# Performance work log

Hardware: AMD Instinct MI355X
Metric: run time of the kernel (lower is better)

Reference implementation:

```python
import jax, jax.numpy as jnp
import numpy as np

B, S, D = 4, 2048, 1024


def setup_inputs() -> dict:
    key = jax.random.key(0)
    k1, k2, k3, k4 = jax.random.split(key, 4)
    x = jax.random.normal(k1, (B, S, D), dtype=jnp.float32)
    # 'random_normal' keras initializer uses stddev=0.05
    w_keys = jax.random.normal(k2, (D, D), dtype=jnp.float32) * 0.05
    w_queries = jax.random.normal(k3, (D, D), dtype=jnp.float32) * 0.05
    w_values = jax.random.normal(k4, (D, D), dtype=jnp.float32) * 0.05
    return {"x": x, "w_keys": w_keys, "w_queries": w_queries, "w_values": w_values}


def reference(x, w_keys, w_queries, w_values):
    # fact = sqrt(input feature dim)
    fact = jnp.sqrt(jnp.asarray(x.shape[-1], x.dtype))
    vk = x @ w_keys      # [B,S,D]
    vq = x @ w_queries   # [B,S,D]
    vv = x @ w_values    # [B,S,D]
    # NOTE: module computes K @ Q^T (keys as rows), softmax over last axis
    kq = jnp.einsum('bsd,btd->bst', vk, vq) / fact   # [B,S,S]
    sn = jax.nn.softmax(kq, axis=-1)
    # pm + transpose_b cancel: out = sn @ vv
    out = jnp.einsum('bst,btd->bsd', sn, vv)         # [B,S,D]
    return out
```

## Files before the change

kernel.cpp:

```cpp
#include <hip/hip_runtime.h>


typedef __attribute__((ext_vector_type(8))) short bf16x8;
typedef __attribute__((ext_vector_type(4))) float f32x4;

__device__ __forceinline__ unsigned short f2bf(float f) {
    unsigned int u = __float_as_uint(f);
    u += 0x7fff + ((u >> 16) & 1);
    return (unsigned short)(u >> 16);
}
__device__ __forceinline__ float bf2f(unsigned short s) {
    return __uint_as_float((unsigned int)s << 16);
}

__device__ __forceinline__ void gld_lds16(const unsigned short* g, unsigned short* l) {
    __builtin_amdgcn_global_load_lds(
        (const __attribute__((address_space(1))) void*)g,
        (__attribute__((address_space(3))) void*)l, 16, 0, 0);
}

template<int N> __device__ __forceinline__ void vmcnt_wait() {
    if constexpr (N == 0) asm volatile("s_waitcnt vmcnt(0)" ::: "memory");
    else if constexpr (N == 8) asm volatile("s_waitcnt vmcnt(8)" ::: "memory");
}
__device__ __forceinline__ void bar() {
    asm volatile("" ::: "memory");
    __builtin_amdgcn_s_barrier();
    asm volatile("" ::: "memory");
}

template<int KT, bool RS>
__device__ __forceinline__ void gemm4(
    const unsigned short* __restrict__ A, const unsigned short* __restrict__ B,
    int lda, int ldb, int bm, int bn,
    unsigned short* As, unsigned short* Bs,
    f32x4 (&acc)[4][4], float (&rs)[4])
{
    const int tid  = threadIdx.x;
    const int lane = tid & 63;
    const int wave = tid >> 6;
    const int wr = wave >> 1, wc = wave & 1;
    const int lr = lane & 15, kg = lane >> 4;

    const int srow = tid >> 2;
    const int ssrc = ((tid & 3) ^ ((tid >> 3) & 3)) * 8;
    const unsigned short* pa0 = A + (size_t)(bm + srow) * lda + ssrc;
    const unsigned short* pa1 = A + (size_t)(bm + 64 + srow) * lda + ssrc;
    const unsigned short* pb0 = B + (size_t)(bn + srow) * ldb + ssrc;
    const unsigned short* pb1 = B + (size_t)(bn + 64 + srow) * ldb + ssrc;

    const int phys = (kg ^ ((lr >> 1) & 3)) * 8;
    const int aoff = (wr * 64 + lr) * 32 + phys;
    const int boff = (wc * 64 + lr) * 32 + phys;

    auto stage = [&](int buf, int kt) {
        unsigned short* da = As + buf * 8192 + wave * 512;
        unsigned short* db = Bs + buf * 8192 + wave * 512;
        #pragma unroll
        for (int kh = 0; kh < 2; kh++) {
            const int go = kt * 64 + kh * 32;
            gld_lds16(pa0 + go, da + kh * 4096);
            gld_lds16(pa1 + go, da + kh * 4096 + 2048);
            gld_lds16(pb0 + go, db + kh * 4096);
            gld_lds16(pb1 + go, db + kh * 4096 + 2048);
        }
    };

    stage(0, 0);
    stage(1, 1);
    vmcnt_wait<8>();
    bar();

    for (int kt = 0; kt < KT; ++kt) {
        const int c = kt & 1;
        const unsigned short* Ab = As + c * 8192 + aoff;
        const unsigned short* Bb = Bs + c * 8192 + boff;

        #pragma unroll
        for (int kh = 0; kh < 2; kh++) {
            bf16x8 af[4], bf[4];
            #pragma unroll
            for (int mf = 0; mf < 4; mf++)
                af[mf] = *reinterpret_cast<const bf16x8*>(Ab + kh * 4096 + mf * 512);
            #pragma unroll
            for (int nf = 0; nf < 4; nf++)
                bf[nf] = *reinterpret_cast<const bf16x8*>(Bb + kh * 4096 + nf * 512);
            __builtin_amdgcn_s_setprio(1);
            #pragma unroll
            for (int mf = 0; mf < 4; mf++)
                #pragma unroll
                for (int nf = 0; nf < 4; nf++)
                    acc[mf][nf] = __builtin_amdgcn_mfma_f32_16x16x32_bf16(af[mf], bf[nf], acc[mf][nf], 0, 0, 0);
            __builtin_amdgcn_s_setprio(0);
            if constexpr (RS) {
                #pragma unroll
                for (int mf = 0; mf < 4; mf++)
                    #pragma unroll
                    for (int e = 0; e < 8; e++) rs[mf] += bf2f(((unsigned short*)&af[mf])[e]);
            }
        }

        if (kt == KT - 1) break;
        bar();
        if (kt + 2 < KT) {
            stage(c, kt + 2);
            vmcnt_wait<8>();
        } else {
            vmcnt_wait<0>();
        }
        bar();
    }
}

__global__ __launch_bounds__(256) void convert_x(
    const float* __restrict__ x, unsigned short* __restrict__ xb)
{
    const size_t idx = (size_t)blockIdx.x * 256 + threadIdx.x;
    const float4* xi = reinterpret_cast<const float4*>(x) + idx * 2;
    float4 v0 = xi[0], v1 = xi[1];
    ushort4 a = { f2bf(v0.x), f2bf(v0.y), f2bf(v0.z), f2bf(v0.w) };
    ushort4 b = { f2bf(v1.x), f2bf(v1.y), f2bf(v1.z), f2bf(v1.w) };
    ushort4* xo = reinterpret_cast<ushort4*>(xb) + idx * 2;
    xo[0] = a; xo[1] = b;
}

__global__ __launch_bounds__(256) void transpose_w(
    const float* __restrict__ w0, const float* __restrict__ w1, const float* __restrict__ w2,
    unsigned short* __restrict__ wT)
{
    __shared__ unsigned short T[64][72];
    const int z = blockIdx.z;
    const float* w = (z == 0) ? w0 : (z == 1 ? w1 : w2);
    unsigned short* o = wT + (size_t)z * 1024 * 1024;
    const int k0 = blockIdx.y * 64, n0 = blockIdx.x * 64;
    const int tid = threadIdx.x;
    const int r = tid >> 4, c4 = (tid & 15) * 4;
    #pragma unroll
    for (int i = 0; i < 4; i++) {
        int kr = r + i * 16;
        float4 v = *reinterpret_cast<const float4*>(&w[(size_t)(k0 + kr) * 1024 + n0 + c4]);
        T[c4 + 0][kr] = f2bf(v.x);
        T[c4 + 1][kr] = f2bf(v.y);
        T[c4 + 2][kr] = f2bf(v.z);
        T[c4 + 3][kr] = f2bf(v.w);
    }
    __syncthreads();
    #pragma unroll
    for (int i = 0; i < 4; i++) {
        int n = r + i * 16;
        ushort4 v = *reinterpret_cast<const ushort4*>(&T[n][c4]);
        *reinterpret_cast<ushort4*>(&o[(size_t)(n0 + n) * 1024 + k0 + c4]) = v;
    }
}

__global__ __launch_bounds__(256, 2) void proj_gemm(
    const unsigned short* __restrict__ xb, const unsigned short* __restrict__ wT,
    unsigned short* __restrict__ vk, unsigned short* __restrict__ vq,
    unsigned short* __restrict__ vvT)
{
    __shared__ unsigned short As[2 * 128 * 64], Bs[2 * 128 * 64];
    const int bid = blockIdx.x;
    const int wg  = (bid & 7) * 192 + (bid >> 3);
    const int z   = wg >> 9;
    const int rem = wg & 511;
    const int bm  = (rem >> 3) * 128;
    const int bn  = (rem & 7) * 128;
    const unsigned short* Bw = wT + (size_t)z * 1024 * 1024;

    f32x4 acc[4][4] = {};
    float rs[4] = {};
    gemm4<16, false>(xb, Bw, 1024, 1024, bm, bn, As, Bs, acc, rs);

    const int tid = threadIdx.x, lane = tid & 63, wave = tid >> 6;
    const int wr = wave >> 1, wc = wave & 1, lr = lane & 15, kg = lane >> 4;
    if (z < 2) {
        unsigned short* out = z ? vq : vk;
        #pragma unroll
        for (int mf = 0; mf < 4; mf++)
            #pragma unroll
            for (int nf = 0; nf < 4; nf++)
                #pragma unroll
                for (int r = 0; r < 4; r++)
                    out[(size_t)(bm + wr * 64 + mf * 16 + kg * 4 + r) * 1024
                        + bn + wc * 64 + nf * 16 + lr] = f2bf(acc[mf][nf][r]);
    } else {
        const int batch = bm >> 11;
        unsigned short* o = vvT + (size_t)batch * 1024 * 2048;
        #pragma unroll
        for (int mf = 0; mf < 4; mf++)
            #pragma unroll
            for (int nf = 0; nf < 4; nf++) {
                ushort4 v = { f2bf(acc[mf][nf][0]), f2bf(acc[mf][nf][1]),
                              f2bf(acc[mf][nf][2]), f2bf(acc[mf][nf][3]) };
                *reinterpret_cast<ushort4*>(
                    &o[(size_t)(bn + wc * 64 + nf * 16 + lr) * 2048
                       + (bm & 2047) + wr * 64 + mf * 16 + kg * 4]) = v;
            }
    }
}

__global__ __launch_bounds__(256, 2) void scores_gemm(
    const unsigned short* __restrict__ vk, const unsigned short* __restrict__ vq,
    unsigned short* __restrict__ P)
{
    __shared__ unsigned short As[2 * 128 * 64], Bs[2 * 128 * 64];
    const int bid = blockIdx.x;
    const int wg  = (bid & 7) * 128 + (bid >> 3);
    const int z   = wg >> 8;
    const int rem = wg & 255;
    const int bm  = (rem >> 4) * 128;
    const int bn  = (rem & 15) * 128;
    const unsigned short* A = vk + (size_t)z * 2048 * 1024;
    const unsigned short* B = vq + (size_t)z * 2048 * 1024;
    unsigned short* out = P + (size_t)z * 2048 * 2048;

    f32x4 acc[4][4] = {};
    float rs[4] = {};
    gemm4<16, false>(A, B, 1024, 1024, bm, bn, As, Bs, acc, rs);

    const int tid = threadIdx.x, lane = tid & 63, wave = tid >> 6;
    const int wr = wave >> 1, wc = wave & 1, lr = lane & 15, kg = lane >> 4;
    #pragma unroll
    for (int mf = 0; mf < 4; mf++)
        #pragma unroll
        for (int nf = 0; nf < 4; nf++)
            #pragma unroll
            for (int r = 0; r < 4; r++)
                out[(size_t)(bm + wr * 64 + mf * 16 + kg * 4 + r) * 2048
                    + bn + wc * 64 + nf * 16 + lr]
                    = f2bf(__expf(acc[mf][nf][r] * 0.03125f));
}

__global__ __launch_bounds__(256, 2) void pv_gemm(
    const unsigned short* __restrict__ P, const unsigned short* __restrict__ vvT,
    float* __restrict__ out)
{
    __shared__ unsigned short As[2 * 128 * 64], Bs[2 * 128 * 64];
    const int bid = blockIdx.x;
    const int wg  = (bid & 7) * 64 + (bid >> 3);
    const int z   = wg >> 7;
    const int rem = wg & 127;
    const int bm  = (rem >> 3) * 128;
    const int bn  = (rem & 7) * 128;
    const unsigned short* A = P   + (size_t)z * 2048 * 2048;
    const unsigned short* B = vvT + (size_t)z * 1024 * 2048;
    float* o = out + (size_t)z * 2048 * 1024;

    f32x4 acc[4][4] = {};
    float rs[4] = {};
    gemm4<32, true>(A, B, 2048, 2048, bm, bn, As, Bs, acc, rs);

    const int tid = threadIdx.x, lane = tid & 63, wave = tid >> 6;
    const int wr = wave >> 1, wc = wave & 1, lr = lane & 15, kg = lane >> 4;

    #pragma unroll
    for (int mf = 0; mf < 4; mf++) {
        rs[mf] += __shfl_xor(rs[mf], 16);
        rs[mf] += __shfl_xor(rs[mf], 32);
    }
    #pragma unroll
    for (int mf = 0; mf < 4; mf++)
        #pragma unroll
        for (int r = 0; r < 4; r++) {
            const float l = __shfl(rs[mf], kg * 4 + r);
            const float inv = 1.0f / l;
            #pragma unroll
            for (int nf = 0; nf < 4; nf++)
                o[(size_t)(bm + wr * 64 + mf * 16 + kg * 4 + r) * 1024
                  + bn + wc * 64 + nf * 16 + lr] = acc[mf][nf][r] * inv;
        }
}

extern "C" void kernel_launch(void* const* d_in, const int* in_sizes, int n_in,
                              void* d_out, int out_size, void* d_ws, size_t ws_size,
                              hipStream_t stream) {
    const float* x  = (const float*)d_in[0];
    const float* wk = (const float*)d_in[1];
    const float* wq = (const float*)d_in[2];
    const float* wv = (const float*)d_in[3];
    float* out = (float*)d_out;

    char* ws = (char*)d_ws;
    const size_t MB = 1024 * 1024;
    unsigned short* xb  = (unsigned short*)(ws);
    unsigned short* wT  = (unsigned short*)(ws + 16 * MB);
    unsigned short* P   = (unsigned short*)(ws);
    unsigned short* vk  = (unsigned short*)(ws + 64 * MB);
    unsigned short* vq  = (unsigned short*)(ws + 80 * MB);
    unsigned short* vvT = (unsigned short*)(ws + 96 * MB);

    convert_x  <<<dim3(4096),      256, 0, stream>>>(x, xb);
    transpose_w<<<dim3(16, 16, 3), 256, 0, stream>>>(wk, wq, wv, wT);
    proj_gemm  <<<dim3(1536),      256, 0, stream>>>(xb, wT, vk, vq, vvT);
    scores_gemm<<<dim3(1024),      256, 0, stream>>>(vk, vq, P);
    pv_gemm    <<<dim3(512),       256, 0, stream>>>(P, vvT, out);
}
```

Baseline: 174.0 us.

## Fold key and query projections into a single precomputed weight product

Uses the identity K Q^T = x (Wk Wq^T) x^T. A small GEMM builds G = Wq·Wk^T (stored as Gt), then y = x·G is formed, and the scores are computed as y·x^T instead of from separate key and query projections. This removes one of the three large projection GEMMs and its 16 MB intermediate, at the cost of a small 1024^3 GEMM, extra conversion launches, and an additional bf16 rounding of G that may change accuracy.

```diff
diff --git a/kernel.cpp b/kernel.cpp
--- a/kernel.cpp
+++ b/kernel.cpp
@@ -112,26 +112,22 @@
     }
 }
 
-__global__ __launch_bounds__(256) void convert_x(
-    const float* __restrict__ x, unsigned short* __restrict__ xb)
+__global__ __launch_bounds__(256) void convert_bf16(
+    const float* __restrict__ src, unsigned short* __restrict__ dst)
 {
     const size_t idx = (size_t)blockIdx.x * 256 + threadIdx.x;
-    const float4* xi = reinterpret_cast<const float4*>(x) + idx * 2;
+    const float4* xi = reinterpret_cast<const float4*>(src) + idx * 2;
     float4 v0 = xi[0], v1 = xi[1];
     ushort4 a = { f2bf(v0.x), f2bf(v0.y), f2bf(v0.z), f2bf(v0.w) };
     ushort4 b = { f2bf(v1.x), f2bf(v1.y), f2bf(v1.z), f2bf(v1.w) };
-    ushort4* xo = reinterpret_cast<ushort4*>(xb) + idx * 2;
+    ushort4* xo = reinterpret_cast<ushort4*>(dst) + idx * 2;
     xo[0] = a; xo[1] = b;
 }
 
-__global__ __launch_bounds__(256) void transpose_w(
-    const float* __restrict__ w0, const float* __restrict__ w1, const float* __restrict__ w2,
-    unsigned short* __restrict__ wT)
+__global__ __launch_bounds__(256) void transpose_w1(
+    const float* __restrict__ w, unsigned short* __restrict__ o)
 {
     __shared__ unsigned short T[64][72];
-    const int z = blockIdx.z;
-    const float* w = (z == 0) ? w0 : (z == 1 ? w1 : w2);
-    unsigned short* o = wT + (size_t)z * 1024 * 1024;
     const int k0 = blockIdx.y * 64, n0 = blockIdx.x * 64;
     const int tid = threadIdx.x;
     const int r = tid >> 4, c4 = (tid & 15) * 4;
@@ -153,19 +149,45 @@
     }
 }
 
-__global__ __launch_bounds__(256, 2) void proj_gemm(
-    const unsigned short* __restrict__ xb, const unsigned short* __restrict__ wT,
-    unsigned short* __restrict__ vk, unsigned short* __restrict__ vq,
-    unsigned short* __restrict__ vvT)
+__global__ __launch_bounds__(256, 2) void g_gemm(
+    const unsigned short* __restrict__ wqb, const unsigned short* __restrict__ wkb,
+    unsigned short* __restrict__ Gt)
 {
     __shared__ unsigned short As[2 * 128 * 64], Bs[2 * 128 * 64];
     const int bid = blockIdx.x;
-    const int wg  = (bid & 7) * 192 + (bid >> 3);
+    const int wg  = (bid & 7) * 8 + (bid >> 3);
+    const int bm  = (wg >> 3) * 128;
+    const int bn  = (wg & 7) * 128;
+
+    f32x4 acc[4][4] = {};
+    float rs[4] = {};
+    gemm4<16, false>(wqb, wkb, 1024, 1024, bm, bn, As, Bs, acc, rs);
+
+    const int tid = threadIdx.x, lane = tid & 63, wave = tid >> 6;
+    const int wr = wave >> 1, wc = wave & 1, lr = lane & 15, kg = lane >> 4;
+    #pragma unroll
+    for (int mf = 0; mf < 4; mf++)
+        #pragma unroll
+        for (int nf = 0; nf < 4; nf++)
+            #pragma unroll
+            for (int r = 0; r < 4; r++)
+                Gt[(size_t)(bm + wr * 64 + mf * 16 + kg * 4 + r) * 1024
+                   + bn + wc * 64 + nf * 16 + lr] = f2bf(acc[mf][nf][r]);
+}
+
+__global__ __launch_bounds__(256, 2) void proj_gemm(
+    const unsigned short* __restrict__ xb, const unsigned short* __restrict__ Gt,
+    const unsigned short* __restrict__ wvT,
+    unsigned short* __restrict__ y, unsigned short* __restrict__ vvT)
+{
+    __shared__ unsigned short As[2 * 128 * 64], Bs[2 * 128 * 64];
+    const int bid = blockIdx.x;
+    const int wg  = (bid & 7) * 128 + (bid >> 3);
     const int z   = wg >> 9;
     const int rem = wg & 511;
     const int bm  = (rem >> 3) * 128;
     const int bn  = (rem & 7) * 128;
-    const unsigned short* Bw = wT + (size_t)z * 1024 * 1024;
+    const unsigned short* Bw = z ? wvT : Gt;
 
     f32x4 acc[4][4] = {};
     float rs[4] = {};
@@ -173,16 +195,15 @@
 
     const int tid = threadIdx.x, lane = tid & 63, wave = tid >> 6;
     const int wr = wave >> 1, wc = wave & 1, lr = lane & 15, kg = lane >> 4;
-    if (z < 2) {
-        unsigned short* out = z ? vq : vk;
+    if (z == 0) {
         #pragma unroll
         for (int mf = 0; mf < 4; mf++)
             #pragma unroll
             for (int nf = 0; nf < 4; nf++)
                 #pragma unroll
                 for (int r = 0; r < 4; r++)
-                    out[(size_t)(bm + wr * 64 + mf * 16 + kg * 4 + r) * 1024
-                        + bn + wc * 64 + nf * 16 + lr] = f2bf(acc[mf][nf][r]);
+                    y[(size_t)(bm + wr * 64 + mf * 16 + kg * 4 + r) * 1024
+                      + bn + wc * 64 + nf * 16 + lr] = f2bf(acc[mf][nf][r]);
     } else {
         const int batch = bm >> 11;
         unsigned short* o = vvT + (size_t)batch * 1024 * 2048;
@@ -200,7 +221,7 @@
 }
 
 __global__ __launch_bounds__(256, 2) void scores_gemm(
-    const unsigned short* __restrict__ vk, const unsigned short* __restrict__ vq,
+    const unsigned short* __restrict__ y, const unsigned short* __restrict__ xb,
     unsigned short* __restrict__ P)
 {
     __shared__ unsigned short As[2 * 128 * 64], Bs[2 * 128 * 64];
@@ -210,8 +231,8 @@
     const int rem = wg & 255;
     const int bm  = (rem >> 4) * 128;
     const int bn  = (rem & 15) * 128;
-    const unsigned short* A = vk + (size_t)z * 2048 * 1024;
-    const unsigned short* B = vq + (size_t)z * 2048 * 1024;
+    const unsigned short* A = y  + (size_t)z * 2048 * 1024;
+    const unsigned short* B = xb + (size_t)z * 2048 * 1024;
     unsigned short* out = P + (size_t)z * 2048 * 2048;
 
     f32x4 acc[4][4] = {};
@@ -283,15 +304,20 @@
     char* ws = (char*)d_ws;
     const size_t MB = 1024 * 1024;
     unsigned short* xb  = (unsigned short*)(ws);
-    unsigned short* wT  = (unsigned short*)(ws + 16 * MB);
-    unsigned short* P   = (unsigned short*)(ws);
-    unsigned short* vk  = (unsigned short*)(ws + 64 * MB);
-    unsigned short* vq  = (unsigned short*)(ws + 80 * MB);
-    unsigned short* vvT = (unsigned short*)(ws + 96 * MB);
-
-    convert_x  <<<dim3(4096),      256, 0, stream>>>(x, xb);
-    transpose_w<<<dim3(16, 16, 3), 256, 0, stream>>>(wk, wq, wv, wT);
-    proj_gemm  <<<dim3(1536),      256, 0, stream>>>(xb, wT, vk, vq, vvT);
-    scores_gemm<<<dim3(1024),      256, 0, stream>>>(vk, vq, P);
-    pv_gemm    <<<dim3(512),       256, 0, stream>>>(P, vvT, out);
-}
+    unsigned short* y   = (unsigned short*)(ws + 16 * MB);
+    unsigned short* wqb = (unsigned short*)(ws + 32 * MB);
+    unsigned short* wkb = (unsigned short*)(ws + 34 * MB);
+    unsigned short* Gt  = (unsigned short*)(ws + 36 * MB);
+    unsigned short* wvT = (unsigned short*)(ws + 38 * MB);
+    unsigned short* vvT = (unsigned short*)(ws + 40 * MB);
+    unsigned short* P   = (unsigned short*)(ws + 56 * MB);
+
+    convert_bf16<<<dim3(4096),     256, 0, stream>>>(x,  xb);
+    convert_bf16<<<dim3(512),      256, 0, stream>>>(wq, wqb);
+    convert_bf16<<<dim3(512),      256, 0, stream>>>(wk, wkb);
+    transpose_w1<<<dim3(16, 16),   256, 0, stream>>>(wv, wvT);
+    g_gemm      <<<dim3(64),       256, 0, stream>>>(wqb, wkb, Gt);
+    proj_gemm   <<<dim3(1024),     256, 0, stream>>>(xb, Gt, wvT, y, vvT);
+    scores_gemm <<<dim3(1024),     256, 0, stream>>>(y, xb, P);
+    pv_gemm     <<<dim3(512),      256, 0, stream>>>(P, vvT, out);
+}
```

New measurement: 172.0 us. No clear change (-1.1%).
